# Kernel tuning notes

Measured on AMD Instinct MI355X. Metric: run time of the kernel, lower is better.

## Reference

```python
import jax, jax.numpy as jnp
import numpy as np

B, C_IN, C_OUT, H, W = 8, 32, 32, 256, 256
M1H, M2H = 32, 32  # modes1//2, modes2//2 (dilate=1)
WSCALE = 0.02      # ~xavier-ish scale for weights


def setup_inputs() -> dict:
    key = jax.random.key(0)
    ks = jax.random.split(key, 6)
    wshape = (C_IN, C_OUT, M1H, M2H)
    return {
        "x": jax.random.normal(ks[0], (B, C_IN, H, W), jnp.float32),
        "w1r": jax.random.normal(ks[1], wshape, jnp.float32) * WSCALE,
        "w1i": jax.random.normal(ks[2], wshape, jnp.float32) * WSCALE,
        "w2r": jax.random.normal(ks[3], wshape, jnp.float32) * WSCALE,
        "w2i": jax.random.normal(ks[4], wshape, jnp.float32) * WSCALE,
        "bias": jax.random.normal(ks[5], (1, C_OUT, 1, 1), jnp.float32),
    }


def reference(x, w1r, w1i, w2r, w2i, bias):
    # complex spectral weights (torch.view_as_complex equivalent)
    w1 = w1r + 1j * w1i  # [I, O, m1h, m2h]
    w2 = w2r + 1j * w2i
    b, c, h, w = x.shape
    x_ft = jnp.fft.rfft2(x)  # [B, I, H, W//2+1] complex64
    # mode-truncated complex channel mixing on low-frequency corners
    out_lo = jnp.einsum('bixy,ioxy->boxy', x_ft[:, :, :M1H, :M2H], w1)
    out_hi = jnp.einsum('bixy,ioxy->boxy', x_ft[:, :, -M1H:, :M2H], w2)
    out_ft = jnp.zeros((b, w1.shape[1], h, w // 2 + 1), jnp.complex64)
    out_ft = out_ft.at[:, :, :M1H, :M2H].set(out_lo)
    out_ft = out_ft.at[:, :, -M1H:, :M2H].set(out_hi)
    out = jnp.fft.irfft2(out_ft, s=(h, w))  # [B, O, H, W] float32
    return out + bias
```

## Files before the change

kernel.cpp:

```cpp
#include <hip/hip_runtime.h>
#include <hip/hip_bf16.h>


#define BD 256

typedef __attribute__((ext_vector_type(8))) short bf16x8;
typedef __attribute__((ext_vector_type(4))) float f32x4;

__device__ inline unsigned short f2bf(float f) {
    union { float f; unsigned u; } v; v.f = f;
    unsigned r = v.u + 0x7FFF + ((v.u >> 16) & 1);
    return (unsigned short)(r >> 16);
}

__global__ void k_setup(float2* __restrict__ tw,
                        unsigned short* __restrict__ BmA, unsigned short* __restrict__ BmC,
                        const float* __restrict__ w1r, const float* __restrict__ w1i,
                        const float* __restrict__ w2r, const float* __restrict__ w2i,
                        float2* __restrict__ wpack) {
    __shared__ float Tr[64][65];
    __shared__ float Ti[64][65];
    int b = blockIdx.x, t = threadIdx.x;
    if (b == 0) {
        double th = 6.283185307179586476925286766559 * (double)t / 256.0;
        tw[t] = make_float2((float)cos(th), (float)sin(th));
    } else if (b <= 128) {
        int idx = (b - 1) * BD + t;
        if (idx < 16384) {
            int w = idx & 255, n = idx >> 8;
            int ky = n >> 1, c = n & 1;
            double th = 6.283185307179586476925286766559 * (double)((ky * w) & 255) / 256.0;
            BmA[idx] = f2bf(c ? (float)(-sin(th)) : (float)cos(th));
        } else {
            int j = idx - 16384;
            int k = j & 63, w = j >> 6;
            int ky = k >> 1, c = k & 1;
            double th = 6.283185307179586476925286766559 * (double)((ky * w) & 255) / 256.0;
            BmC[j] = f2bf(c ? (float)(-sin(th)) : (float)cos(th));
        }
    } else {
        int blk = b - 129;
        int half = blk >> 8;
        int tile = blk & 255;
        int tr = tile >> 4, tc = tile & 15;
        int io0 = tr * 64, cm0 = tc * 64;
        const float* wr = half ? w2r : w1r;
        const float* wi = half ? w2i : w1i;
        int rr = t >> 2, c0 = (t & 3) * 16;
        {
            const float4* srcr = (const float4*)(wr + (long)(io0 + rr) * 1024 + cm0 + c0);
            const float4* srci = (const float4*)(wi + (long)(io0 + rr) * 1024 + cm0 + c0);
#pragma unroll
            for (int p = 0; p < 4; ++p) {
                float4 vr = srcr[p], vi = srci[p];
                int cc = c0 + p * 4;
                Tr[rr][cc + 0] = vr.x; Tr[rr][cc + 1] = vr.y; Tr[rr][cc + 2] = vr.z; Tr[rr][cc + 3] = vr.w;
                Ti[rr][cc + 0] = vi.x; Ti[rr][cc + 1] = vi.y; Ti[rr][cc + 2] = vi.z; Ti[rr][cc + 3] = vi.w;
            }
        }
        __syncthreads();
        {
            int cm = cm0 + rr;
            int ky = cm & 31;
            float s = (ky == 0 ? 1.0f : 2.0f) * (1.0f / 65536.0f);
            float2* dst = wpack + ((long)(half * 1024 + cm)) * 1024 + io0 + c0;
#pragma unroll
            for (int k = 0; k < 16; ++k)
                dst[k] = make_float2(Tr[c0 + k][rr] * s, Ti[c0 + k][rr] * s);
        }
    }
}

__global__ __launch_bounds__(512) void k_fftA(const float* __restrict__ x,
                                              const unsigned short* __restrict__ BmA,
                                              const float2* __restrict__ tw,
                                              float2* __restrict__ Z) {
    __shared__ __align__(16) unsigned short Bs[64 * 264];
    __shared__ __align__(16) unsigned short As[32 * 264];
    __shared__ __align__(16) float Ys[32 * 64];
    int t = threadIdx.x, bi = blockIdx.x;
    {
        int n = t >> 3, c0 = (t & 7) * 32;
        const uint4* src = (const uint4*)(BmA + n * 256 + c0);
        unsigned short* dst = &Bs[n * 264 + c0];
#pragma unroll
        for (int j = 0; j < 4; ++j) *(uint4*)(dst + j * 8) = src[j];
    }
    int sr = t >> 4, sc = (t & 15) * 16;
    const float* xrow = x + ((long)bi * 256 + sr) * 256 + sc;
    float4 xb[4];
#pragma unroll
    for (int j = 0; j < 4; ++j) xb[j] = *(const float4*)(xrow + j * 4);
    {
        unsigned short* dst = &As[sr * 264 + sc];
#pragma unroll
        for (int j = 0; j < 4; ++j) {
            float4 v = xb[j]; ushort4 bq;
            bq.x = f2bf(v.x); bq.y = f2bf(v.y); bq.z = f2bf(v.z); bq.w = f2bf(v.w);
            *(ushort4*)(dst + j * 4) = bq;
        }
    }
    __syncthreads();
    int wv = t >> 6, lane = t & 63, lm = lane & 15, quad = lane >> 4;
    int mh = wv & 1, nq = wv >> 1;
    int kxi = t & 63, g = wv;
    int kxv = (kxi < 32) ? kxi : kxi + 192;
    float2 st = tw[kxv];
    float C = st.x, S = st.y;
    float zr[4] = {0.f, 0.f, 0.f, 0.f}, zi[4] = {0.f, 0.f, 0.f, 0.f};
    for (int c = 0; c < 8; ++c) {
        f32x4 acc = {};
#pragma unroll
        for (int kk = 0; kk < 8; ++kk) {
            bf16x8 af = *(const bf16x8*)&As[(mh * 16 + lm) * 264 + kk * 32 + quad * 8];
            bf16x8 bf = *(const bf16x8*)&Bs[(nq * 16 + lm) * 264 + kk * 32 + quad * 8];
            acc = __builtin_amdgcn_mfma_f32_16x16x32_bf16(af, bf, acc, 0, 0, 0);
        }
        if (c < 7) {
            const float* xr = xrow + (c + 1) * 32 * 256;
#pragma unroll
            for (int j = 0; j < 4; ++j) xb[j] = *(const float4*)(xr + j * 4);
        }
#pragma unroll
        for (int r = 0; r < 4; ++r)
            Ys[(mh * 16 + quad * 4 + r) * 64 + nq * 16 + lm] = acc[r];
        __syncthreads();
        float2 cw = tw[(kxv * (c * 32)) & 255];
        float cr = cw.x, ci = cw.y;
        for (int hh = 0; hh < 32; ++hh) {
            float4 y0 = *(const float4*)&Ys[hh * 64 + g * 8];
            float4 y1 = *(const float4*)&Ys[hh * 64 + g * 8 + 4];
            zr[0] = fmaf(y0.x, cr, fmaf(y0.y,  ci, zr[0]));
            zi[0] = fmaf(y0.y, cr, fmaf(-y0.x, ci, zi[0]));
            zr[1] = fmaf(y0.z, cr, fmaf(y0.w,  ci, zr[1]));
            zi[1] = fmaf(y0.w, cr, fmaf(-y0.z, ci, zi[1]));
            zr[2] = fmaf(y1.x, cr, fmaf(y1.y,  ci, zr[2]));
            zi[2] = fmaf(y1.y, cr, fmaf(-y1.x, ci, zi[2]));
            zr[3] = fmaf(y1.z, cr, fmaf(y1.w,  ci, zr[3]));
            zi[3] = fmaf(y1.w, cr, fmaf(-y1.z, ci, zi[3]));
            float nc = fmaf(cr, C, -ci * S);
            ci = fmaf(ci, C, cr * S);
            cr = nc;
        }
        if (c < 7) {
            unsigned short* dst = &As[sr * 264 + sc];
#pragma unroll
            for (int j = 0; j < 4; ++j) {
                float4 v = xb[j]; ushort4 bq;
                bq.x = f2bf(v.x); bq.y = f2bf(v.y); bq.z = f2bf(v.z); bq.w = f2bf(v.w);
                *(ushort4*)(dst + j * 4) = bq;
            }
        }
        __syncthreads();
    }
    float2* Zo = (float2*)As;
    {
#pragma unroll
        for (int j = 0; j < 4; ++j)
            Zo[kxi * 32 + g * 4 + j] = make_float2(zr[j], zi[j]);
    }
    __syncthreads();
    {
        float4* dst = (float4*)(Z + (long)bi * 2048);
        const float4* src = (const float4*)Zo;
        dst[t] = src[t];
        dst[t + 512] = src[t + 512];
    }
}

__global__ void k_mix(const float2* __restrict__ Z, const float2* __restrict__ wpack,
                      float2* __restrict__ Zmix) {
    __shared__ float2 Ws[4][1024];
    __shared__ float2 Zs[256][4];
    __shared__ float2 Os[256][4];
    int t = threadIdx.x;
    int mk0 = blockIdx.x * 4;
    {
        const float4* src = (const float4*)(wpack + (long)mk0 * 1024);
        float4* dst = (float4*)&Ws[0][0];
        for (int j = t; j < 2048; j += BD) dst[j] = src[j];
    }
    for (int j = t; j < 512; j += BD) {
        int bi = j >> 1, p = j & 1;
        *(float4*)&Zs[bi][p * 2] = *(const float4*)&Z[(long)bi * 2048 + mk0 + p * 2];
    }
    __syncthreads();
    int o = t & 31, kk = (t >> 5) & 3, bh = t >> 7;
    float ar[4], ai[4];
#pragma unroll
    for (int j = 0; j < 4; ++j) { ar[j] = 0.f; ai[j] = 0.f; }
    for (int i = 0; i < 32; ++i) {
        float2 w = Ws[kk][i * 32 + o];
#pragma unroll
        for (int j = 0; j < 4; ++j) {
            float2 z = Zs[(bh * 4 + j) * 32 + i][kk];
            ar[j] = fmaf(z.x, w.x, fmaf(-z.y, w.y, ar[j]));
            ai[j] = fmaf(z.x, w.y, fmaf( z.y, w.x, ai[j]));
        }
    }
#pragma unroll
    for (int j = 0; j < 4; ++j)
        Os[(bh * 4 + j) * 32 + o][kk] = make_float2(ar[j], ai[j]);
    __syncthreads();
    for (int j = t; j < 512; j += BD) {
        int row = j >> 1, p = j & 1;
        *(float4*)&Zmix[(long)row * 2048 + mk0 + p * 2] = *(float4*)&Os[row][p * 2];
    }
}

__global__ __launch_bounds__(256) void k_fftC(const float2* __restrict__ Zmix,
                                              const float2* __restrict__ tw,
                                              const unsigned short* __restrict__ BmC,
                                              const float* __restrict__ bias,
                                              float* __restrict__ out) {
    __shared__ __align__(16) unsigned short Gs[128 * 72];
    __shared__ __align__(16) char buf[128 * 72 * 2];
    int t = threadIdx.x;
    int bo = blockIdx.x >> 1, hb = blockIdx.x & 1;
    float2* Zs = (float2*)buf;
    unsigned short* Bsh = (unsigned short*)buf;
    {
        const float4* src = (const float4*)(Zmix + (long)bo * 2048);
        float4* dst = (float4*)Zs;
#pragma unroll
        for (int p = 0; p < 4; ++p) dst[t + p * 256] = src[t + p * 256];
    }
    __syncthreads();
    int h1 = t & 127, yh = t >> 7;
    int h = hb * 128 + h1;
    float2 st = tw[h];
    float C = st.x, S = st.y;
    float gr[16], gi[16];
#pragma unroll
    for (int k = 0; k < 16; ++k) { gr[k] = 0.f; gi[k] = 0.f; }
    float cr = 1.f, ci = 0.f;
    for (int hf = 0; hf < 2; ++hf) {
        if (hf) { float2 s2 = tw[(224 * h) & 255]; cr = s2.x; ci = s2.y; }
        for (int mm = 0; mm < 32; ++mm) {
            int m = hf * 32 + mm;
#pragma unroll
            for (int kk = 0; kk < 8; ++kk) {
                float4 z = *(const float4*)&Zs[m * 32 + yh * 16 + kk * 2];
                gr[kk*2]   = fmaf(z.x, cr, fmaf(-z.y, ci, gr[kk*2]));
                gi[kk*2]   = fmaf(z.y, cr, fmaf( z.x, ci, gi[kk*2]));
                gr[kk*2+1] = fmaf(z.z, cr, fmaf(-z.w, ci, gr[kk*2+1]));
                gi[kk*2+1] = fmaf(z.w, cr, fmaf( z.z, ci, gi[kk*2+1]));
            }
            float nc = fmaf(cr, C, -ci * S);
            ci = fmaf(ci, C, cr * S);
            cr = nc;
        }
    }
    {
        unsigned* Gp = (unsigned*)&Gs[h1 * 72 + yh * 32];
#pragma unroll
        for (int k = 0; k < 16; ++k)
            Gp[k] = (unsigned)f2bf(gr[k]) | ((unsigned)f2bf(gi[k]) << 16);
    }
    __syncthreads();
    int wv = t >> 6, lane = t & 63, m = lane & 15, quad = lane >> 4;
    bf16x8 a[2][2];
#pragma unroll
    for (int ms = 0; ms < 2; ++ms)
#pragma unroll
        for (int kh = 0; kh < 2; ++kh)
            a[ms][kh] = *(const bf16x8*)&Gs[(wv * 32 + ms * 16 + m) * 72 + kh * 32 + quad * 8];
    float bv = bias[bo & 31];
    long rowbase = (long)bo * 256 + hb * 128 + wv * 32;
    for (int p = 0; p < 2; ++p) {
        {
            int w = t >> 1, k0 = (t & 1) * 32;
            const uint4* src = (const uint4*)(BmC + (p * 128 + w) * 64 + k0);
            unsigned short* dst = &Bsh[w * 72 + k0];
#pragma unroll
            for (int j = 0; j < 4; ++j) *(uint4*)(dst + j * 8) = src[j];
        }
        __syncthreads();
        f32x4 acc[16] = {};
#pragma unroll
        for (int nt = 0; nt < 8; ++nt) {
            bf16x8 b0 = *(const bf16x8*)&Bsh[(nt * 16 + m) * 72 + quad * 8];
            bf16x8 b1 = *(const bf16x8*)&Bsh[(nt * 16 + m) * 72 + 32 + quad * 8];
#pragma unroll
            for (int ms = 0; ms < 2; ++ms) {
                acc[ms * 8 + nt] = __builtin_amdgcn_mfma_f32_16x16x32_bf16(a[ms][0], b0, acc[ms * 8 + nt], 0, 0, 0);
                acc[ms * 8 + nt] = __builtin_amdgcn_mfma_f32_16x16x32_bf16(a[ms][1], b1, acc[ms * 8 + nt], 0, 0, 0);
            }
        }
#pragma unroll
        for (int ms = 0; ms < 2; ++ms)
#pragma unroll
            for (int nt = 0; nt < 8; ++nt)
#pragma unroll
                for (int r = 0; r < 4; ++r)
                    out[(rowbase + ms * 16 + quad * 4 + r) * 256 + p * 128 + nt * 16 + m] = acc[ms * 8 + nt][r] + bv;
        __syncthreads();
    }
}

extern "C" void kernel_launch(void* const* d_in, const int* in_sizes, int n_in,
                              void* d_out, int out_size, void* d_ws, size_t ws_size,
                              hipStream_t stream) {
    const float* x    = (const float*)d_in[0];
    const float* w1r  = (const float*)d_in[1];
    const float* w1i  = (const float*)d_in[2];
    const float* w2r  = (const float*)d_in[3];
    const float* w2i  = (const float*)d_in[4];
    const float* bias = (const float*)d_in[5];

    char* ws = (char*)d_ws;
    float2* tw             = (float2*)(ws);
    float2* wpack          = (float2*)(ws + 4096);
    unsigned short* BmA    = (unsigned short*)(ws + 4096 + (16l << 20));
    unsigned short* BmC    = BmA + 64 * 256;
    float2* Z              = (float2*)(ws + 4096 + (16l << 20) + 65536);
    float2* Zmix           = (float2*)((char*)Z + (4l << 20));
    float* out             = (float*)d_out;

    k_setup <<<1 + 128 + 512, BD, 0, stream>>>(tw, BmA, BmC, w1r, w1i, w2r, w2i, wpack);
    k_fftA  <<<256, 512, 0, stream>>>(x, BmA, tw, Z);
    k_mix   <<<512, BD, 0, stream>>>(Z, wpack, Zmix);
    k_fftC  <<<512, BD, 0, stream>>>(Zmix, tw, BmC, bias, out);
}
```

Measured before the change: 190.6 us.

## Split forward FFT over row halves and double fftC threads per block

The forward-transform kernel now launches two blocks per image-channel, each covering half the rows and writing a partial spectrum. The mixing kernel sums the two partials when it loads them. The inverse kernel runs 512 threads per block, so each thread accumulates half as many columns and each wave handles 16 rows instead of 32. This raises parallelism and occupancy on a 256-CU GPU, at the cost of twice the intermediate Z traffic and an extra add in the mixing kernel.

```diff
diff --git a/kernel.cpp b/kernel.cpp
--- a/kernel.cpp
+++ b/kernel.cpp
@@ -78,7 +78,7 @@
     __shared__ __align__(16) unsigned short Bs[64 * 264];
     __shared__ __align__(16) unsigned short As[32 * 264];
     __shared__ __align__(16) float Ys[32 * 64];
-    int t = threadIdx.x, bi = blockIdx.x;
+    int t = threadIdx.x, bi = blockIdx.x >> 1, hh2 = blockIdx.x & 1;
     {
         int n = t >> 3, c0 = (t & 7) * 32;
         const uint4* src = (const uint4*)(BmA + n * 256 + c0);
@@ -87,7 +87,7 @@
         for (int j = 0; j < 4; ++j) *(uint4*)(dst + j * 8) = src[j];
     }
     int sr = t >> 4, sc = (t & 15) * 16;
-    const float* xrow = x + ((long)bi * 256 + sr) * 256 + sc;
+    const float* xrow = x + ((long)bi * 256 + hh2 * 128 + sr) * 256 + sc;
     float4 xb[4];
 #pragma unroll
     for (int j = 0; j < 4; ++j) xb[j] = *(const float4*)(xrow + j * 4);
@@ -108,7 +108,7 @@
     float2 st = tw[kxv];
     float C = st.x, S = st.y;
     float zr[4] = {0.f, 0.f, 0.f, 0.f}, zi[4] = {0.f, 0.f, 0.f, 0.f};
-    for (int c = 0; c < 8; ++c) {
+    for (int c2 = 0; c2 < 4; ++c2) {
         f32x4 acc = {};
 #pragma unroll
         for (int kk = 0; kk < 8; ++kk) {
@@ -116,8 +116,8 @@
             bf16x8 bf = *(const bf16x8*)&Bs[(nq * 16 + lm) * 264 + kk * 32 + quad * 8];
             acc = __builtin_amdgcn_mfma_f32_16x16x32_bf16(af, bf, acc, 0, 0, 0);
         }
-        if (c < 7) {
-            const float* xr = xrow + (c + 1) * 32 * 256;
+        if (c2 < 3) {
+            const float* xr = xrow + (c2 + 1) * 32 * 256;
 #pragma unroll
             for (int j = 0; j < 4; ++j) xb[j] = *(const float4*)(xr + j * 4);
         }
@@ -125,7 +125,8 @@
         for (int r = 0; r < 4; ++r)
             Ys[(mh * 16 + quad * 4 + r) * 64 + nq * 16 + lm] = acc[r];
         __syncthreads();
-        float2 cw = tw[(kxv * (c * 32)) & 255];
+        int gc = hh2 * 4 + c2;
+        float2 cw = tw[(kxv * (gc * 32)) & 255];
         float cr = cw.x, ci = cw.y;
         for (int hh = 0; hh < 32; ++hh) {
             float4 y0 = *(const float4*)&Ys[hh * 64 + g * 8];
@@ -142,7 +143,7 @@
             ci = fmaf(ci, C, cr * S);
             cr = nc;
         }
-        if (c < 7) {
+        if (c2 < 3) {
             unsigned short* dst = &As[sr * 264 + sc];
 #pragma unroll
             for (int j = 0; j < 4; ++j) {
@@ -161,7 +162,7 @@
     }
     __syncthreads();
     {
-        float4* dst = (float4*)(Z + (long)bi * 2048);
+        float4* dst = (float4*)(Z + (long)(hh2 * 256 + bi) * 2048);
         const float4* src = (const float4*)Zo;
         dst[t] = src[t];
         dst[t + 512] = src[t + 512];
@@ -182,7 +183,11 @@
     }
     for (int j = t; j < 512; j += BD) {
         int bi = j >> 1, p = j & 1;
-        *(float4*)&Zs[bi][p * 2] = *(const float4*)&Z[(long)bi * 2048 + mk0 + p * 2];
+        float4 a = *(const float4*)&Z[(long)bi * 2048 + mk0 + p * 2];
+        float4 b = *(const float4*)&Z[(long)(256 + bi) * 2048 + mk0 + p * 2];
+        float4 s;
+        s.x = a.x + b.x; s.y = a.y + b.y; s.z = a.z + b.z; s.w = a.w + b.w;
+        *(float4*)&Zs[bi][p * 2] = s;
     }
     __syncthreads();
     int o = t & 31, kk = (t >> 5) & 3, bh = t >> 7;
@@ -208,7 +213,7 @@
     }
 }
 
-__global__ __launch_bounds__(256) void k_fftC(const float2* __restrict__ Zmix,
+__global__ __launch_bounds__(512) void k_fftC(const float2* __restrict__ Zmix,
                                               const float2* __restrict__ tw,
                                               const unsigned short* __restrict__ BmC,
                                               const float* __restrict__ bias,
@@ -222,25 +227,25 @@
     {
         const float4* src = (const float4*)(Zmix + (long)bo * 2048);
         float4* dst = (float4*)Zs;
-#pragma unroll
-        for (int p = 0; p < 4; ++p) dst[t + p * 256] = src[t + p * 256];
+        dst[t] = src[t];
+        dst[t + 512] = src[t + 512];
     }
     __syncthreads();
     int h1 = t & 127, yh = t >> 7;
     int h = hb * 128 + h1;
     float2 st = tw[h];
     float C = st.x, S = st.y;
-    float gr[16], gi[16];
-#pragma unroll
-    for (int k = 0; k < 16; ++k) { gr[k] = 0.f; gi[k] = 0.f; }
+    float gr[8], gi[8];
+#pragma unroll
+    for (int k = 0; k < 8; ++k) { gr[k] = 0.f; gi[k] = 0.f; }
     float cr = 1.f, ci = 0.f;
     for (int hf = 0; hf < 2; ++hf) {
         if (hf) { float2 s2 = tw[(224 * h) & 255]; cr = s2.x; ci = s2.y; }
         for (int mm = 0; mm < 32; ++mm) {
             int m = hf * 32 + mm;
 #pragma unroll
-            for (int kk = 0; kk < 8; ++kk) {
-                float4 z = *(const float4*)&Zs[m * 32 + yh * 16 + kk * 2];
+            for (int kk = 0; kk < 4; ++kk) {
+                float4 z = *(const float4*)&Zs[m * 32 + yh * 8 + kk * 2];
                 gr[kk*2]   = fmaf(z.x, cr, fmaf(-z.y, ci, gr[kk*2]));
                 gi[kk*2]   = fmaf(z.y, cr, fmaf( z.x, ci, gi[kk*2]));
                 gr[kk*2+1] = fmaf(z.z, cr, fmaf(-z.w, ci, gr[kk*2+1]));
@@ -252,49 +257,39 @@
         }
     }
     {
-        unsigned* Gp = (unsigned*)&Gs[h1 * 72 + yh * 32];
-#pragma unroll
-        for (int k = 0; k < 16; ++k)
+        unsigned* Gp = (unsigned*)&Gs[h1 * 72 + yh * 16];
+#pragma unroll
+        for (int k = 0; k < 8; ++k)
             Gp[k] = (unsigned)f2bf(gr[k]) | ((unsigned)f2bf(gi[k]) << 16);
     }
     __syncthreads();
     int wv = t >> 6, lane = t & 63, m = lane & 15, quad = lane >> 4;
-    bf16x8 a[2][2];
-#pragma unroll
-    for (int ms = 0; ms < 2; ++ms)
-#pragma unroll
-        for (int kh = 0; kh < 2; ++kh)
-            a[ms][kh] = *(const bf16x8*)&Gs[(wv * 32 + ms * 16 + m) * 72 + kh * 32 + quad * 8];
+    bf16x8 a0 = *(const bf16x8*)&Gs[(wv * 16 + m) * 72 + quad * 8];
+    bf16x8 a1 = *(const bf16x8*)&Gs[(wv * 16 + m) * 72 + 32 + quad * 8];
     float bv = bias[bo & 31];
-    long rowbase = (long)bo * 256 + hb * 128 + wv * 32;
+    long rowbase = (long)bo * 256 + hb * 128 + wv * 16;
     for (int p = 0; p < 2; ++p) {
+        if (p) __syncthreads();
         {
-            int w = t >> 1, k0 = (t & 1) * 32;
+            int w = t >> 2, k0 = (t & 3) * 16;
             const uint4* src = (const uint4*)(BmC + (p * 128 + w) * 64 + k0);
-            unsigned short* dst = &Bsh[w * 72 + k0];
-#pragma unroll
-            for (int j = 0; j < 4; ++j) *(uint4*)(dst + j * 8) = src[j];
+            *(uint4*)&Bsh[w * 72 + k0]     = src[0];
+            *(uint4*)&Bsh[w * 72 + k0 + 8] = src[1];
         }
         __syncthreads();
-        f32x4 acc[16] = {};
+        f32x4 acc[8] = {};
 #pragma unroll
         for (int nt = 0; nt < 8; ++nt) {
             bf16x8 b0 = *(const bf16x8*)&Bsh[(nt * 16 + m) * 72 + quad * 8];
             bf16x8 b1 = *(const bf16x8*)&Bsh[(nt * 16 + m) * 72 + 32 + quad * 8];
-#pragma unroll
-            for (int ms = 0; ms < 2; ++ms) {
-                acc[ms * 8 + nt] = __builtin_amdgcn_mfma_f32_16x16x32_bf16(a[ms][0], b0, acc[ms * 8 + nt], 0, 0, 0);
-                acc[ms * 8 + nt] = __builtin_amdgcn_mfma_f32_16x16x32_bf16(a[ms][1], b1, acc[ms * 8 + nt], 0, 0, 0);
-            }
-        }
-#pragma unroll
-        for (int ms = 0; ms < 2; ++ms)
-#pragma unroll
-            for (int nt = 0; nt < 8; ++nt)
-#pragma unroll
-                for (int r = 0; r < 4; ++r)
-                    out[(rowbase + ms * 16 + quad * 4 + r) * 256 + p * 128 + nt * 16 + m] = acc[ms * 8 + nt][r] + bv;
-        __syncthreads();
+            acc[nt] = __builtin_amdgcn_mfma_f32_16x16x32_bf16(a0, b0, acc[nt], 0, 0, 0);
+            acc[nt] = __builtin_amdgcn_mfma_f32_16x16x32_bf16(a1, b1, acc[nt], 0, 0, 0);
+        }
+#pragma unroll
+        for (int nt = 0; nt < 8; ++nt)
+#pragma unroll
+            for (int r = 0; r < 4; ++r)
+                out[(rowbase + quad * 4 + r) * 256 + p * 128 + nt * 16 + m] = acc[nt][r] + bv;
     }
 }
 
@@ -314,11 +309,11 @@
     unsigned short* BmA    = (unsigned short*)(ws + 4096 + (16l << 20));
     unsigned short* BmC    = BmA + 64 * 256;
     float2* Z              = (float2*)(ws + 4096 + (16l << 20) + 65536);
-    float2* Zmix           = (float2*)((char*)Z + (4l << 20));
+    float2* Zmix           = (float2*)((char*)Z + (8l << 20));
     float* out             = (float*)d_out;
 
     k_setup <<<1 + 128 + 512, BD, 0, stream>>>(tw, BmA, BmC, w1r, w1i, w2r, w2i, wpack);
-    k_fftA  <<<256, 512, 0, stream>>>(x, BmA, tw, Z);
+    k_fftA  <<<512, 512, 0, stream>>>(x, BmA, tw, Z);
     k_mix   <<<512, BD, 0, stream>>>(Z, wpack, Zmix);
-    k_fftC  <<<512, BD, 0, stream>>>(Zmix, tw, BmC, bias, out);
-}
+    k_fftC  <<<512, 512, 0, stream>>>(Zmix, tw, BmC, bias, out);
+}
```

Result: no change. 194.3 us (+2.0%).
